# Kernel optimization log

Hardware: AMD Instinct MI355X
Metric: run time of the kernel (lower is better)

Reference implementation:

```python
import jax, jax.numpy as jnp
import numpy as np

N_NODES = 100000
N_EDGES = 3200000
IN_FEATS = 7
HIDDEN = 32


def setup_inputs() -> dict:
    key = jax.random.key(0)
    ks = jax.random.split(key, 9)
    inp = {
        "x_t": jax.random.normal(ks[0], (N_NODES, IN_FEATS), dtype=jnp.float32),
        "x_t_dt": jax.random.normal(ks[1], (N_NODES, IN_FEATS), dtype=jnp.float32),
        "edge_index": jax.random.randint(ks[2], (2, N_EDGES), 0, N_NODES, dtype=jnp.int64),
        # node_encoder: Linear(in_feats, hidden)
        "W_enc": jax.random.normal(ks[3], (IN_FEATS, HIDDEN), dtype=jnp.float32) * 0.1,
        "b_enc": jnp.zeros((HIDDEN,), dtype=jnp.float32),
        # GCNConv(hidden, hidden): weight + bias
        "W_gcn": jax.random.normal(ks[4], (HIDDEN, HIDDEN), dtype=jnp.float32) * 0.1,
        "b_gcn": jnp.zeros((HIDDEN,), dtype=jnp.float32),
        # edge_classifier: Linear(2*hidden, 1)
        "W_edge": jax.random.normal(ks[5], (2 * HIDDEN, 1), dtype=jnp.float32) * 0.1,
        "b_edge": jnp.zeros((1,), dtype=jnp.float32),
    }
    return inp


def reference(x_t, x_t_dt, edge_index, W_enc, b_enc, W_gcn, b_gcn, W_edge, b_edge):
    N = x_t.shape[0]
    src, dst = edge_index[0], edge_index[1]

    # node encoder + relu
    h = jax.nn.relu(x_t @ W_enc + b_enc)

    # GCNConv (PyG default): add self-loops, symmetric normalization
    h = h @ W_gcn  # [N, H]
    deg = jax.ops.segment_sum(jnp.ones(src.shape[0], h.dtype), dst, num_segments=N) + 1.0
    dinv = jax.lax.rsqrt(deg)  # deg^-1/2, [N]
    norm = dinv[src] * dinv[dst]  # [E]
    agg = jax.ops.segment_sum(h[src] * norm[:, None], dst, num_segments=N)
    # self-loop contribution: dinv[i]*dinv[i]*h[i]
    h = agg + h * (dinv * dinv)[:, None] + b_gcn
    h = jax.nn.relu(h)
    # dropout: identity in eval mode

    # edge scorer: gather src/dst, concat, linear, sigmoid
    edge_repr = jnp.concatenate([h[src], h[dst]], axis=-1)  # [E, 2H]
    scores = jax.nn.sigmoid(edge_repr @ W_edge + b_edge).reshape(-1)  # [E]
    return scores
```

## Files before the change

kernel.cpp:

```cpp
#include <hip/hip_runtime.h>
#include <hip/hip_fp16.h>
#include <math.h>

#define NN 100000
#define NE 3200000
#define IN_F 7
#define H 32

#define BSH 9
#define BSPAN 512
#define NBUK ((NN + BSPAN - 1) / BSPAN)
#define EPB 8192

__global__ __launch_bounds__(256) void k_encode(const float* __restrict__ x,
                                                const float* __restrict__ Wenc,
                                                const float* __restrict__ benc,
                                                const float* __restrict__ Wgcn,
                                                uint4* __restrict__ hW_h4) {
    __shared__ float sWe[IN_F * H];
    __shared__ float sb[H];
    __shared__ float sWg[H * H];
    for (int i = threadIdx.x; i < IN_F * H; i += 256) sWe[i] = Wenc[i];
    for (int i = threadIdx.x; i < H; i += 256) sb[i] = benc[i];
    for (int i = threadIdx.x; i < H * H; i += 256) sWg[i] = Wgcn[i];
    __syncthreads();

    int n = blockIdx.x * 256 + threadIdx.x;
    if (n >= NN) return;

    float xl[IN_F];
#pragma unroll
    for (int j = 0; j < IN_F; ++j) xl[j] = x[n * IN_F + j];

    float h[H];
#pragma unroll
    for (int k = 0; k < H; ++k) {
        float a = sb[k];
#pragma unroll
        for (int j = 0; j < IN_F; ++j) a = fmaf(xl[j], sWe[j * H + k], a);
        h[k] = fmaxf(a, 0.f);
    }
    float a[H];
#pragma unroll
    for (int k = 0; k < H; ++k) {
        float s = 0.f;
#pragma unroll
        for (int j = 0; j < H; ++j) s = fmaf(h[j], sWg[j * H + k], s);
        a[k] = s;
    }
    uint4 pk[4];
    __half2* hp = reinterpret_cast<__half2*>(pk);
#pragma unroll
    for (int k = 0; k < 16; ++k) hp[k] = __floats2half2_rn(a[2 * k], a[2 * k + 1]);
#pragma unroll
    for (int q = 0; q < 4; ++q) hW_h4[n * 4 + q] = pk[q];
}

__global__ __launch_bounds__(1024) void k_bhist(const int* __restrict__ dst,
                                                int* __restrict__ bucket_cnt) {
    __shared__ int cnt[NBUK];
    for (int i = threadIdx.x; i < NBUK; i += 1024) cnt[i] = 0;
    __syncthreads();
    int base = blockIdx.x * EPB;
#pragma unroll
    for (int r = 0; r < EPB / 1024; ++r) {
        int e = base + r * 1024 + threadIdx.x;
        if (e < NE) atomicAdd(&cnt[dst[e] >> BSH], 1);
    }
    __syncthreads();
    for (int i = threadIdx.x; i < NBUK; i += 1024)
        if (cnt[i]) atomicAdd(&bucket_cnt[i], cnt[i]);
}

__global__ __launch_bounds__(256) void k_bscan(const int* __restrict__ bucket_cnt,
                                               int* __restrict__ bucket_base,
                                               int* __restrict__ bucket_cur) {
    __shared__ int tmp[256];
    int t = threadIdx.x;
    int v = (t < NBUK) ? bucket_cnt[t] : 0;
    tmp[t] = v;
    __syncthreads();
    for (int off = 1; off < 256; off <<= 1) {
        int u = (t >= off) ? tmp[t - off] : 0;
        __syncthreads();
        tmp[t] += u;
        __syncthreads();
    }
    int ex = tmp[t] - v;
    if (t < NBUK) {
        bucket_base[t] = ex;
        bucket_cur[t] = ex;
    }
    if (t == NBUK - 1) bucket_base[NBUK] = ex + v;
}

__global__ __launch_bounds__(1024) void k_bscatter(const int* __restrict__ src,
                                                   const int* __restrict__ dst,
                                                   int* __restrict__ bucket_cur,
                                                   unsigned int* __restrict__ pairs) {
    __shared__ int cnt[NBUK];
    __shared__ int cbase[NBUK];
    for (int i = threadIdx.x; i < NBUK; i += 1024) cnt[i] = 0;
    __syncthreads();
    int base = blockIdx.x * EPB;
#pragma unroll
    for (int r = 0; r < EPB / 1024; ++r) {
        int e = base + r * 1024 + threadIdx.x;
        if (e < NE) atomicAdd(&cnt[dst[e] >> BSH], 1);
    }
    __syncthreads();
    for (int i = threadIdx.x; i < NBUK; i += 1024) {
        int c = cnt[i];
        cbase[i] = c ? atomicAdd(&bucket_cur[i], c) : 0;
    }
    __syncthreads();
    for (int i = threadIdx.x; i < NBUK; i += 1024) cnt[i] = 0;
    __syncthreads();
#pragma unroll
    for (int r = 0; r < EPB / 1024; ++r) {
        int e = base + r * 1024 + threadIdx.x;
        if (e < NE) {
            int d = dst[e];
            int b = d >> BSH;
            int lp = atomicAdd(&cnt[b], 1);
            pairs[cbase[b] + lp] = ((unsigned int)src[e] << BSH) | (unsigned int)(d & (BSPAN - 1));
        }
    }
}

__global__ __launch_bounds__(1024) void k_bfill(const unsigned int* __restrict__ pairs,
                                                const int* __restrict__ bucket_base,
                                                int* __restrict__ row_ptr,
                                                float* __restrict__ dinv,
                                                int* __restrict__ csr_src) {
    __shared__ int cnt[BSPAN];
    __shared__ int pre[BSPAN];
    int b = blockIdx.x;
    int ebeg = bucket_base[b], eend = bucket_base[b + 1];
    int t = threadIdx.x;
    for (int i = t; i < BSPAN; i += 1024) cnt[i] = 0;
    __syncthreads();
    for (int e = ebeg + t; e < eend; e += 1024)
        atomicAdd(&cnt[pairs[e] & (BSPAN - 1)], 1);
    __syncthreads();
    if (t < BSPAN) pre[t] = cnt[t];
    __syncthreads();
    for (int off = 1; off < BSPAN; off <<= 1) {
        int v = (t < BSPAN && t >= off) ? pre[t - off] : 0;
        __syncthreads();
        if (t < BSPAN) pre[t] += v;
        __syncthreads();
    }
    int nbase = b * BSPAN;
    if (t < BSPAN) {
        int node = nbase + t;
        if (node < NN) {
            row_ptr[node] = ebeg + pre[t] - cnt[t];
            dinv[node] = rsqrtf((float)cnt[t] + 1.0f);
        }
    }
    if (b == NBUK - 1 && t == 0) row_ptr[NN] = NE;
    __syncthreads();
    if (t < BSPAN) cnt[t] = ebeg + pre[t] - cnt[t];
    __syncthreads();
    for (int e = ebeg + t; e < eend; e += 1024) {
        unsigned int p = pairs[e];
        int pos = atomicAdd(&cnt[p & (BSPAN - 1)], 1);
        csr_src[pos] = (int)(p >> BSH);
    }
}

__global__ __launch_bounds__(256) void k_gather(const int* __restrict__ row_ptr,
                                                const int* __restrict__ csr_src,
                                                const float* __restrict__ dinv,
                                                const uint4* __restrict__ hW_h4,
                                                const float* __restrict__ bgcn,
                                                const float* __restrict__ We,
                                                float2* __restrict__ ab) {
    int tid = blockIdx.x * 256 + threadIdx.x;
    int n = tid >> 2;
    int c = tid & 3;
    if (n >= NN) return;
    float dn = dinv[n];
    int beg = row_ptr[n], end = row_ptr[n + 1];
    float acc[8];
#pragma unroll
    for (int i = 0; i < 8; ++i) acc[i] = 0.f;
    for (int k = beg; k < end; ++k) {
        int s = csr_src[k];
        float nrm = dinv[s] * dn;
        uint4 v = hW_h4[s * 4 + c];
        const __half2* hp = reinterpret_cast<const __half2*>(&v);
#pragma unroll
        for (int i = 0; i < 4; ++i) {
            float2 f = __half22float2(hp[i]);
            acc[2 * i]     = fmaf(f.x, nrm, acc[2 * i]);
            acc[2 * i + 1] = fmaf(f.y, nrm, acc[2 * i + 1]);
        }
    }
    float sl = dn * dn;
    uint4 w = hW_h4[n * 4 + c];
    const __half2* wp = reinterpret_cast<const __half2*>(&w);
    float dota = 0.f, dotb = 0.f;
#pragma unroll
    for (int i = 0; i < 4; ++i) {
        float2 f = __half22float2(wp[i]);
        float r0 = fmaxf(acc[2 * i]     + f.x * sl + bgcn[c * 8 + 2 * i],     0.f);
        float r1 = fmaxf(acc[2 * i + 1] + f.y * sl + bgcn[c * 8 + 2 * i + 1], 0.f);
        dota = fmaf(r0, We[c * 8 + 2 * i],         dota);
        dota = fmaf(r1, We[c * 8 + 2 * i + 1],     dota);
        dotb = fmaf(r0, We[H + c * 8 + 2 * i],     dotb);
        dotb = fmaf(r1, We[H + c * 8 + 2 * i + 1], dotb);
    }
    dota += __shfl_xor(dota, 1, 4);
    dota += __shfl_xor(dota, 2, 4);
    dotb += __shfl_xor(dotb, 1, 4);
    dotb += __shfl_xor(dotb, 2, 4);
    if (c == 0) ab[n] = make_float2(dota, dotb);
}

__global__ __launch_bounds__(256) void k_edge(const int* __restrict__ src,
                                              const int* __restrict__ dst,
                                              const float2* __restrict__ ab,
                                              const float* __restrict__ be,
                                              float* __restrict__ out) {
    int e = blockIdx.x * 256 + threadIdx.x;
    if (e >= NE) return;
    float logit = ab[src[e]].x + ab[dst[e]].y + be[0];
    float sc = 1.0f / (1.0f + __expf(-logit));
    __builtin_nontemporal_store(sc, &out[e]);
}

extern "C" void kernel_launch(void* const* d_in, const int* in_sizes, int n_in,
                              void* d_out, int out_size, void* d_ws, size_t ws_size,
                              hipStream_t stream) {
    const float* x_t   = (const float*)d_in[0];
    const int*   eidx  = (const int*)d_in[2];
    const float* Wenc  = (const float*)d_in[3];
    const float* benc  = (const float*)d_in[4];
    const float* Wgcn  = (const float*)d_in[5];
    const float* bgcn  = (const float*)d_in[6];
    const float* Wedge = (const float*)d_in[7];
    const float* bedge = (const float*)d_in[8];
    float* out = (float*)d_out;

    const int* src = eidx;
    const int* dst = eidx + NE;

    char* ws = (char*)d_ws;
    if (ws_size < 33700000) return;

    uint4*        hW_h4    = (uint4*)(ws);
    unsigned int* pairs    = (unsigned int*)(ws + 6400064);
    int*          csr_src  = (int*)(ws + 19200128);
    int*          row_ptr  = (int*)(ws + 32000192);
    float*        dinv     = (float*)(ws + 32400256);
    float2*       ab       = (float2*)(ws + 32800320);
    int*          bucket_cnt  = (int*)(ws + 33600384);
    int*          bucket_base = (int*)(ws + 33601344);
    int*          bucket_cur  = (int*)(ws + 33602368);

    hipMemsetAsync(bucket_cnt, 0, NBUK * sizeof(int), stream);

    int ebks = (NE + EPB - 1) / EPB;
    k_encode<<<(NN + 255) / 256, 256, 0, stream>>>(x_t, Wenc, benc, Wgcn, hW_h4);
    k_bhist<<<ebks, 1024, 0, stream>>>(dst, bucket_cnt);
    k_bscan<<<1, 256, 0, stream>>>(bucket_cnt, bucket_base, bucket_cur);
    k_bscatter<<<ebks, 1024, 0, stream>>>(src, dst, bucket_cur, pairs);
    k_bfill<<<NBUK, 1024, 0, stream>>>(pairs, bucket_base, row_ptr, dinv, csr_src);
    k_gather<<<(NN * 4 + 255) / 256, 256, 0, stream>>>(row_ptr, csr_src, dinv, hW_h4, bgcn, Wedge, ab);
    k_edge<<<(NE + 255) / 256, 256, 0, stream>>>(src, dst, ab, bedge, out);
}
```

Measured before the change: 265.6 us.

## Pre-scale features by dinv and split gather into two half-width passes

The encoder now runs after the CSR build, so it can multiply each node's transformed features by dinv before storing them. This removes the per-edge dinv[src] lookup and multiply from the gather. The fp16 feature table is split into two 16-channel halves (lo/hi), each gathered by a separate kernel pass so every pass touches a 3.2MB table that fits in cache better. The edge kernel then sums two partial logit arrays, at the cost of reading csr_src twice and an extra launch and partial-sum read.

```diff
diff --git a/kernel.cpp b/kernel.cpp
--- a/kernel.cpp
+++ b/kernel.cpp
@@ -11,50 +11,6 @@
 #define BSPAN 512
 #define NBUK ((NN + BSPAN - 1) / BSPAN)
 #define EPB 8192
-
-__global__ __launch_bounds__(256) void k_encode(const float* __restrict__ x,
-                                                const float* __restrict__ Wenc,
-                                                const float* __restrict__ benc,
-                                                const float* __restrict__ Wgcn,
-                                                uint4* __restrict__ hW_h4) {
-    __shared__ float sWe[IN_F * H];
-    __shared__ float sb[H];
-    __shared__ float sWg[H * H];
-    for (int i = threadIdx.x; i < IN_F * H; i += 256) sWe[i] = Wenc[i];
-    for (int i = threadIdx.x; i < H; i += 256) sb[i] = benc[i];
-    for (int i = threadIdx.x; i < H * H; i += 256) sWg[i] = Wgcn[i];
-    __syncthreads();
-
-    int n = blockIdx.x * 256 + threadIdx.x;
-    if (n >= NN) return;
-
-    float xl[IN_F];
-#pragma unroll
-    for (int j = 0; j < IN_F; ++j) xl[j] = x[n * IN_F + j];
-
-    float h[H];
-#pragma unroll
-    for (int k = 0; k < H; ++k) {
-        float a = sb[k];
-#pragma unroll
-        for (int j = 0; j < IN_F; ++j) a = fmaf(xl[j], sWe[j * H + k], a);
-        h[k] = fmaxf(a, 0.f);
-    }
-    float a[H];
-#pragma unroll
-    for (int k = 0; k < H; ++k) {
-        float s = 0.f;
-#pragma unroll
-        for (int j = 0; j < H; ++j) s = fmaf(h[j], sWg[j * H + k], s);
-        a[k] = s;
-    }
-    uint4 pk[4];
-    __half2* hp = reinterpret_cast<__half2*>(pk);
-#pragma unroll
-    for (int k = 0; k < 16; ++k) hp[k] = __floats2half2_rn(a[2 * k], a[2 * k + 1]);
-#pragma unroll
-    for (int q = 0; q < 4; ++q) hW_h4[n * 4 + q] = pk[q];
-}
 
 __global__ __launch_bounds__(1024) void k_bhist(const int* __restrict__ dst,
                                                 int* __restrict__ bucket_cnt) {
@@ -170,16 +126,68 @@
     }
 }
 
-__global__ __launch_bounds__(256) void k_gather(const int* __restrict__ row_ptr,
-                                                const int* __restrict__ csr_src,
+__global__ __launch_bounds__(256) void k_encode(const float* __restrict__ x,
+                                                const float* __restrict__ Wenc,
+                                                const float* __restrict__ benc,
+                                                const float* __restrict__ Wgcn,
                                                 const float* __restrict__ dinv,
-                                                const uint4* __restrict__ hW_h4,
-                                                const float* __restrict__ bgcn,
-                                                const float* __restrict__ We,
-                                                float2* __restrict__ ab) {
+                                                uint4* __restrict__ lo,
+                                                uint4* __restrict__ hi) {
+    __shared__ float sWe[IN_F * H];
+    __shared__ float sb[H];
+    __shared__ float sWg[H * H];
+    for (int i = threadIdx.x; i < IN_F * H; i += 256) sWe[i] = Wenc[i];
+    for (int i = threadIdx.x; i < H; i += 256) sb[i] = benc[i];
+    for (int i = threadIdx.x; i < H * H; i += 256) sWg[i] = Wgcn[i];
+    __syncthreads();
+
+    int n = blockIdx.x * 256 + threadIdx.x;
+    if (n >= NN) return;
+
+    float xl[IN_F];
+#pragma unroll
+    for (int j = 0; j < IN_F; ++j) xl[j] = x[n * IN_F + j];
+
+    float h[H];
+#pragma unroll
+    for (int k = 0; k < H; ++k) {
+        float a = sb[k];
+#pragma unroll
+        for (int j = 0; j < IN_F; ++j) a = fmaf(xl[j], sWe[j * H + k], a);
+        h[k] = fmaxf(a, 0.f);
+    }
+    float dn = dinv[n];
+    float a[H];
+#pragma unroll
+    for (int k = 0; k < H; ++k) {
+        float s = 0.f;
+#pragma unroll
+        for (int j = 0; j < H; ++j) s = fmaf(h[j], sWg[j * H + k], s);
+        a[k] = s * dn;
+    }
+    uint4 pk[2];
+    __half2* hp = reinterpret_cast<__half2*>(pk);
+#pragma unroll
+    for (int k = 0; k < 8; ++k) hp[k] = __floats2half2_rn(a[2 * k], a[2 * k + 1]);
+    lo[n * 2 + 0] = pk[0];
+    lo[n * 2 + 1] = pk[1];
+#pragma unroll
+    for (int k = 0; k < 8; ++k) hp[k] = __floats2half2_rn(a[16 + 2 * k], a[16 + 2 * k + 1]);
+    hi[n * 2 + 0] = pk[0];
+    hi[n * 2 + 1] = pk[1];
+}
+
+__global__ __launch_bounds__(256) void k_gather_p(const int* __restrict__ row_ptr,
+                                                  const int* __restrict__ csr_src,
+                                                  const float* __restrict__ dinv,
+                                                  const uint4* __restrict__ tab,
+                                                  const float* __restrict__ bg16,
+                                                  const float* __restrict__ we_s,
+                                                  const float* __restrict__ we_d,
+                                                  float2* __restrict__ abp) {
     int tid = blockIdx.x * 256 + threadIdx.x;
-    int n = tid >> 2;
-    int c = tid & 3;
+    int n = tid >> 1;
+    int c = tid & 1;
     if (n >= NN) return;
     float dn = dinv[n];
     int beg = row_ptr[n], end = row_ptr[n + 1];
@@ -188,45 +196,44 @@
     for (int i = 0; i < 8; ++i) acc[i] = 0.f;
     for (int k = beg; k < end; ++k) {
         int s = csr_src[k];
-        float nrm = dinv[s] * dn;
-        uint4 v = hW_h4[s * 4 + c];
+        uint4 v = tab[s * 2 + c];
         const __half2* hp = reinterpret_cast<const __half2*>(&v);
 #pragma unroll
         for (int i = 0; i < 4; ++i) {
             float2 f = __half22float2(hp[i]);
-            acc[2 * i]     = fmaf(f.x, nrm, acc[2 * i]);
-            acc[2 * i + 1] = fmaf(f.y, nrm, acc[2 * i + 1]);
+            acc[2 * i]     += f.x;
+            acc[2 * i + 1] += f.y;
         }
     }
-    float sl = dn * dn;
-    uint4 w = hW_h4[n * 4 + c];
+    uint4 w = tab[n * 2 + c];
     const __half2* wp = reinterpret_cast<const __half2*>(&w);
     float dota = 0.f, dotb = 0.f;
 #pragma unroll
     for (int i = 0; i < 4; ++i) {
         float2 f = __half22float2(wp[i]);
-        float r0 = fmaxf(acc[2 * i]     + f.x * sl + bgcn[c * 8 + 2 * i],     0.f);
-        float r1 = fmaxf(acc[2 * i + 1] + f.y * sl + bgcn[c * 8 + 2 * i + 1], 0.f);
-        dota = fmaf(r0, We[c * 8 + 2 * i],         dota);
-        dota = fmaf(r1, We[c * 8 + 2 * i + 1],     dota);
-        dotb = fmaf(r0, We[H + c * 8 + 2 * i],     dotb);
-        dotb = fmaf(r1, We[H + c * 8 + 2 * i + 1], dotb);
-    }
-    dota += __shfl_xor(dota, 1, 4);
-    dota += __shfl_xor(dota, 2, 4);
-    dotb += __shfl_xor(dotb, 1, 4);
-    dotb += __shfl_xor(dotb, 2, 4);
-    if (c == 0) ab[n] = make_float2(dota, dotb);
+        float r0 = fmaxf(fmaf(dn, acc[2 * i]     + f.x, bg16[c * 8 + 2 * i]),     0.f);
+        float r1 = fmaxf(fmaf(dn, acc[2 * i + 1] + f.y, bg16[c * 8 + 2 * i + 1]), 0.f);
+        dota = fmaf(r0, we_s[c * 8 + 2 * i],     dota);
+        dota = fmaf(r1, we_s[c * 8 + 2 * i + 1], dota);
+        dotb = fmaf(r0, we_d[c * 8 + 2 * i],     dotb);
+        dotb = fmaf(r1, we_d[c * 8 + 2 * i + 1], dotb);
+    }
+    dota += __shfl_xor(dota, 1, 2);
+    dotb += __shfl_xor(dotb, 1, 2);
+    if (c == 0) abp[n] = make_float2(dota, dotb);
 }
 
 __global__ __launch_bounds__(256) void k_edge(const int* __restrict__ src,
                                               const int* __restrict__ dst,
-                                              const float2* __restrict__ ab,
+                                              const float2* __restrict__ ab0,
+                                              const float2* __restrict__ ab1,
                                               const float* __restrict__ be,
                                               float* __restrict__ out) {
     int e = blockIdx.x * 256 + threadIdx.x;
     if (e >= NE) return;
-    float logit = ab[src[e]].x + ab[dst[e]].y + be[0];
+    int s = src[e];
+    int d = dst[e];
+    float logit = ab0[s].x + ab1[s].x + ab0[d].y + ab1[d].y + be[0];
     float sc = 1.0f / (1.0f + __expf(-logit));
     __builtin_nontemporal_store(sc, &out[e]);
 }
@@ -248,26 +255,31 @@
     const int* dst = eidx + NE;
 
     char* ws = (char*)d_ws;
-    if (ws_size < 33700000) return;
-
-    uint4*        hW_h4    = (uint4*)(ws);
-    unsigned int* pairs    = (unsigned int*)(ws + 6400064);
-    int*          csr_src  = (int*)(ws + 19200128);
-    int*          row_ptr  = (int*)(ws + 32000192);
-    float*        dinv     = (float*)(ws + 32400256);
-    float2*       ab       = (float2*)(ws + 32800320);
-    int*          bucket_cnt  = (int*)(ws + 33600384);
-    int*          bucket_base = (int*)(ws + 33601344);
-    int*          bucket_cur  = (int*)(ws + 33602368);
+    if (ws_size < 34500000) return;
+
+    uint4*        lo       = (uint4*)(ws);
+    uint4*        hi       = (uint4*)(ws + 3200000);
+    unsigned int* pairs    = (unsigned int*)(ws + 6400000);
+    int*          csr_src  = (int*)(ws + 19200000);
+    int*          row_ptr  = (int*)(ws + 32000000);
+    float*        dinv     = (float*)(ws + 32400064);
+    float2*       ab0      = (float2*)(ws + 32800064);
+    float2*       ab1      = (float2*)(ws + 33600064);
+    int*          bucket_cnt  = (int*)(ws + 34400064);
+    int*          bucket_base = (int*)(ws + 34401024);
+    int*          bucket_cur  = (int*)(ws + 34402048);
 
     hipMemsetAsync(bucket_cnt, 0, NBUK * sizeof(int), stream);
 
     int ebks = (NE + EPB - 1) / EPB;
-    k_encode<<<(NN + 255) / 256, 256, 0, stream>>>(x_t, Wenc, benc, Wgcn, hW_h4);
     k_bhist<<<ebks, 1024, 0, stream>>>(dst, bucket_cnt);
     k_bscan<<<1, 256, 0, stream>>>(bucket_cnt, bucket_base, bucket_cur);
     k_bscatter<<<ebks, 1024, 0, stream>>>(src, dst, bucket_cur, pairs);
     k_bfill<<<NBUK, 1024, 0, stream>>>(pairs, bucket_base, row_ptr, dinv, csr_src);
-    k_gather<<<(NN * 4 + 255) / 256, 256, 0, stream>>>(row_ptr, csr_src, dinv, hW_h4, bgcn, Wedge, ab);
-    k_edge<<<(NE + 255) / 256, 256, 0, stream>>>(src, dst, ab, bedge, out);
-}
+    k_encode<<<(NN + 255) / 256, 256, 0, stream>>>(x_t, Wenc, benc, Wgcn, dinv, lo, hi);
+    k_gather_p<<<(NN * 2 + 255) / 256, 256, 0, stream>>>(row_ptr, csr_src, dinv, lo,
+                                                         bgcn, Wedge, Wedge + H, ab0);
+    k_gather_p<<<(NN * 2 + 255) / 256, 256, 0, stream>>>(row_ptr, csr_src, dinv, hi,
+                                                         bgcn + 16, Wedge + 16, Wedge + H + 16, ab1);
+    k_edge<<<(NE + 255) / 256, 256, 0, stream>>>(src, dst, ab0, ab1, bedge, out);
+}
```

Result: slower. 318.3 us (+19.8%).
